# Performance work log

Hardware: AMD Instinct MI355X
Metric: run time of the kernel (lower is better)

The kernel has to match this reference:

```python
import jax, jax.numpy as jnp
import numpy as np

B, C, EMB, W, H = 4, 128, 16, 64, 64


def setup_inputs() -> dict:
    key = jax.random.key(0)
    ks = jax.random.split(key, 8)
    return {
        "x": jax.random.normal(ks[0], (B, C, W, H), dtype=jnp.float32),
        "Wq": jax.random.normal(ks[1], (EMB, C), dtype=jnp.float32) * (1.0 / np.sqrt(C)),
        "bq": jax.random.normal(ks[2], (EMB,), dtype=jnp.float32) * 0.01,
        "Wk": jax.random.normal(ks[3], (EMB, C), dtype=jnp.float32) * (1.0 / np.sqrt(C)),
        "bk": jax.random.normal(ks[4], (EMB,), dtype=jnp.float32) * 0.01,
        "Wv": jax.random.normal(ks[5], (C, C), dtype=jnp.float32) * (1.0 / np.sqrt(C)),
        "bv": jax.random.normal(ks[6], (C,), dtype=jnp.float32) * 0.01,
        "gamma": jax.random.normal(ks[7], (1,), dtype=jnp.float32),
    }


def reference(x, Wq, bq, Wk, bk, Wv, bv, gamma):
    b, c, w, h = x.shape
    n = w * h
    xf = x.reshape(b, c, n)  # flatten spatial: [b, c, n]
    # 1x1 convs == per-pixel linear maps
    q = jnp.einsum('ec,bcn->bne', Wq, xf) + bq                # [b, n, emb]
    k = jnp.einsum('ec,bcn->ben', Wk, xf) + bk[:, None]       # [b, emb, n]
    energy = jnp.einsum('bne,bem->bnm', q, k)                 # [b, n, n] (unscaled)
    attn = jax.nn.softmax(energy, axis=-1)                    # softmax over keys m
    v = jnp.einsum('dc,bcn->bdn', Wv, xf) + bv[:, None]       # [b, c, n]
    # torch: out = bmm(V, attn^T) -> out[b,d,n] = sum_m V[b,d,m] * attn[b,n,m]
    out = jnp.einsum('bdm,bnm->bdn', v, attn)
    out = (gamma * out + xf).reshape(b, c, w, h)
    return out
```

## Files before the change

kernel.cpp:

```cpp
#include <hip/hip_runtime.h>


#define NTILE 64
#define PEXP(s) exp2f(fmaf((s), 1.44269504f, -23.08312065f))

typedef __attribute__((ext_vector_type(8))) short bf16x8;
typedef __attribute__((ext_vector_type(4))) float f32x4;
typedef __attribute__((ext_vector_type(4))) int i32x4;

__device__ __forceinline__ bf16x8 asbf(i32x4 v) {
  return __builtin_bit_cast(bf16x8, v);
}
__device__ __forceinline__ int cvtpk(float lo, float hi) {
  int r;
  asm("v_cvt_pk_bf16_f32 %0, %1, %2" : "=v"(r) : "v"(lo), "v"(hi));
  return r;
}
__device__ __forceinline__ float lo16f(int u) {
  return __uint_as_float(((unsigned)u) << 16);
}
__device__ __forceinline__ float hi16f(int u) {
  return __uint_as_float(((unsigned)u) & 0xffff0000u);
}


__global__ __launch_bounds__(256, 4) void proj_kernel(
    const float* __restrict__ xg, const float* __restrict__ Wq,
    const float* __restrict__ bq, const float* __restrict__ Wk,
    const float* __restrict__ bk, const float* __restrict__ Wv,
    const float* __restrict__ bv, char* __restrict__ Qg,
    char* __restrict__ Kg, char* __restrict__ Vg) {
  __shared__ float wlds[10240];
  const int bid = blockIdx.x;
  const int pt = bid & 127, dh = (bid >> 7) & 1, b = bid >> 8;
  const int n0 = pt << 5;
  const int tid = threadIdx.x;

  const float* Wqk = dh ? Wk : Wq;
  for (int i = tid; i < 2560; i += 256) {
    int row = i >> 5, c4 = (i & 31) << 2;
    const float* src = (row < 64) ? (Wv + (size_t)(dh * 64 + row) * 128 + c4)
                                  : (Wqk + (size_t)(row - 64) * 128 + c4);
    *(f32x4*)&wlds[row * 128 + c4] = *(const f32x4*)src;
  }
  __syncthreads();

  const int px = tid & 31, og = tid >> 5;
  const float* xb = xg + (size_t)b * 524288 + n0 + px;

  float av[8];
#pragma unroll
  for (int r = 0; r < 8; r++) av[r] = 0.f;
  float aq[4] = {0.f, 0.f, 0.f, 0.f};

  for (int c0 = 0; c0 < 128; c0 += 4) {
    float x0 = xb[(size_t)(c0 + 0) * 4096];
    float x1 = xb[(size_t)(c0 + 1) * 4096];
    float x2 = xb[(size_t)(c0 + 2) * 4096];
    float x3 = xb[(size_t)(c0 + 3) * 4096];
#pragma unroll
    for (int r = 0; r < 8; r++) {
      const float* wr = &wlds[(og * 8 + r) * 128 + c0];
      av[r] += wr[0] * x0 + wr[1] * x1 + wr[2] * x2 + wr[3] * x3;
    }
    if (og < 4) {
#pragma unroll
      for (int ee = 0; ee < 4; ee++) {
        const float* wr = &wlds[(64 + og * 4 + ee) * 128 + c0];
        aq[ee] += wr[0] * x0 + wr[1] * x1 + wr[2] * x2 + wr[3] * x3;
      }
    }
  }

  if (og < 4) {
    const float* bqk = dh ? bk : bq;
    float v0 = aq[0] + bqk[og * 4 + 0], v1 = aq[1] + bqk[og * 4 + 1];
    float v2 = aq[2] + bqk[og * 4 + 2], v3 = aq[3] + bqk[og * 4 + 3];
    int h0 = cvtpk(v0, v1), h1 = cvtpk(v2, v3);
    float r0 = v0 - lo16f(h0), r1 = v1 - hi16f(h0);
    float r2 = v2 - lo16f(h1), r3 = v3 - hi16f(h1);
    int l0 = cvtpk(r0, r1), l1 = cvtpk(r2, r3);
    i32x4 ch = {h0, h1, l0, l1};
    char* QKg = dh ? Kg : Qg;
    *(i32x4*)(QKg + ((size_t)(b * 16384 + og * 4096 + n0 + px)) * 16) = ch;
  }

  const int d0 = dh * 64 + og * 8;
#pragma unroll
  for (int r = 0; r < 8; r++) av[r] += bv[d0 + r];
  __syncthreads();
#pragma unroll
  for (int r = 0; r < 8; r++) wlds[(og * 8 + r) * 32 + px] = av[r];
  __syncthreads();

  char* vg_t = Vg + (size_t)b * 2097152 + (size_t)(pt >> 1) * 32768;
#pragma unroll
  for (int k = 0; k < 2; k++) {
    int pid = tid + k * 256;
    int gs = pid & 3, d1 = (pid >> 2) & 63, kcl = pid >> 8;
    int d = dh * 64 + d1;
    int gg = gs ^ ((d >> 1) & 3);
    f32x4 v = *(const f32x4*)&wlds[d1 * 32 + kcl * 16 + gg * 4];
    int h0 = cvtpk(v[0], v[1]), h1 = cvtpk(v[2], v[3]);
    float r0 = v[0] - lo16f(h0), r1 = v[1] - hi16f(h0);
    float r2 = v[2] - lo16f(h1), r3 = v[3] - hi16f(h1);
    int l0 = cvtpk(r0, r1), l1 = cvtpk(r2, r3);
    i32x4 ch = {h0, h1, l0, l1};
    int kc = (pt & 1) * 2 + kcl;
    *(i32x4*)(vg_t + ((size_t)((kc * 128 + d) * 4 + gs)) * 16) = ch;
  }
}

__global__ __launch_bounds__(512, 2) void flash_kernel(
    const char* __restrict__ Qg, const char* __restrict__ Kg,
    const char* __restrict__ Vg, const float* __restrict__ xg,
    const float* __restrict__ gammag, float* __restrict__ outg) {
  __shared__ float red_O[64 * 129];
  __shared__ float red_L[64];

  const int bid = blockIdx.x;
  const int xcd = bid & 7, slot2 = bid >> 3;
  const int b = xcd >> 1;
  const int nt = (slot2 << 1) | (xcd & 1);
  const int n0 = nt << 6;

  const int tid = threadIdx.x;
  const int l = tid & 63, w = tid >> 6;
  const int c = l & 15, g = l >> 4;
  const int kc = w & 3, dh = w >> 2;

  const char* kg_b = Kg + (size_t)b * 262144;
  const char* vg_b = Vg + (size_t)b * 2097152;

  const char* vlane =
      vg_b + ((size_t)(kc * 512 + dh * 256 + c * 4 + (g ^ ((c >> 1) & 3)))) * 16;

  const int krow = kc * 16 + c;
  i32x4 kcur = *(const i32x4*)(kg_b + ((size_t)(g * 4096 + krow)) * 16);
  i32x4 qf[4];
#pragma unroll
  for (int qt = 0; qt < 4; qt++) {
    int n = n0 + qt * 16 + c;
    qf[qt] = *(const i32x4*)(Qg + ((size_t)(b * 16384 + g * 4096 + n)) * 16);
  }

  i32x4 vc0 = *(const i32x4*)(vlane + 0);
  i32x4 vc1 = *(const i32x4*)(vlane + 1024);
  i32x4 vc2 = *(const i32x4*)(vlane + 2048);
  i32x4 vc3 = *(const i32x4*)(vlane + 3072);

  const f32x4 zero4 = {0.f, 0.f, 0.f, 0.f};
  f32x4 acc[4][4];
#pragma unroll
  for (int qt = 0; qt < 4; qt++)
#pragma unroll
    for (int dt = 0; dt < 4; dt++) acc[qt][dt] = zero4;
  float lsum[4] = {0.f, 0.f, 0.f, 0.f};

  for (int t = 0; t < NTILE; t++) {
    i32x4 knext = kcur, vn0 = vc0, vn1 = vc1, vn2 = vc2, vn3 = vc3;
    if (t + 1 < NTILE) {
      const char* vnb = vlane + (size_t)(t + 1) * 32768;
      vn0 = *(const i32x4*)(vnb + 0);
      vn1 = *(const i32x4*)(vnb + 1024);
      vn2 = *(const i32x4*)(vnb + 2048);
      vn3 = *(const i32x4*)(vnb + 3072);
      knext = *(const i32x4*)(kg_b +
                              ((size_t)(g * 4096 + (t + 1) * 64 + krow)) * 16);
    }

    i32x4 k2 = {kcur[2], kcur[3], kcur[0], kcur[1]};
    f32x4 st[4];
    __builtin_amdgcn_s_setprio(1);
#pragma unroll
    for (int qt = 0; qt < 4; qt++) {
      f32x4 s = __builtin_amdgcn_mfma_f32_16x16x32_bf16(asbf(kcur), asbf(qf[qt]),
                                                        zero4, 0, 0, 0);
      st[qt] = __builtin_amdgcn_mfma_f32_16x16x32_bf16(asbf(k2), asbf(qf[qt]), s,
                                                       0, 0, 0);
    }
    __builtin_amdgcn_s_setprio(0);

    bf16x8 af[4];
#pragma unroll
    for (int qt = 0; qt < 4; qt++) {
      float p0 = PEXP(st[qt][0]);
      float p1 = PEXP(st[qt][1]);
      float p2 = PEXP(st[qt][2]);
      float p3 = PEXP(st[qt][3]);
      lsum[qt] += (p0 + p1) + (p2 + p3);
      int h0 = cvtpk(p0, p1), h1 = cvtpk(p2, p3);
      i32x4 A = {h0, h1, h0, h1};
      af[qt] = asbf(A);
    }

    __builtin_amdgcn_s_setprio(1);
#pragma unroll
    for (int qt = 0; qt < 4; qt++) {
      acc[qt][0] = __builtin_amdgcn_mfma_f32_16x16x32_bf16(af[qt], asbf(vc0),
                                                           acc[qt][0], 0, 0, 0);
      acc[qt][1] = __builtin_amdgcn_mfma_f32_16x16x32_bf16(af[qt], asbf(vc1),
                                                           acc[qt][1], 0, 0, 0);
      acc[qt][2] = __builtin_amdgcn_mfma_f32_16x16x32_bf16(af[qt], asbf(vc2),
                                                           acc[qt][2], 0, 0, 0);
      acc[qt][3] = __builtin_amdgcn_mfma_f32_16x16x32_bf16(af[qt], asbf(vc3),
                                                           acc[qt][3], 0, 0, 0);
    }
    __builtin_amdgcn_s_setprio(0);

    kcur = knext;
    vc0 = vn0; vc1 = vn1; vc2 = vn2; vc3 = vn3;
  }

  for (int i = tid; i < 64 * 129; i += 512) red_O[i] = 0.f;
  if (tid < 64) red_L[tid] = 0.f;
  __syncthreads();

#pragma unroll
  for (int qt = 0; qt < 4; qt++) {
    float s = lsum[qt];
    s += __shfl_xor(s, 16);
    s += __shfl_xor(s, 32);
    if (g == 0 && dh == 0) atomicAdd(&red_L[qt * 16 + c], s);
#pragma unroll
    for (int dt = 0; dt < 4; dt++) {
#pragma unroll
      for (int i = 0; i < 4; i++) {
        atomicAdd(&red_O[(qt * 16 + 4 * g + i) * 129 + dh * 64 + dt * 16 + c],
                  acc[qt][dt][i]);
      }
    }
  }
  __syncthreads();

  const float gam = gammag[0];
#pragma unroll
  for (int k = 0; k < 4; k++) {
    int id = tid + k * 512;
    int q4 = id & 15, d = id >> 4;
    int q0 = q4 * 4;
    size_t base = ((size_t)(b * 128 + d)) * 4096 + n0 + q0;
    f32x4 x4 = *(const f32x4*)(xg + base);
    f32x4 o;
#pragma unroll
    for (int j = 0; j < 4; j++)
      o[j] = gam * (red_O[(q0 + j) * 129 + d] / red_L[q0 + j]) + x4[j];
    *(f32x4*)(outg + base) = o;
  }
}

extern "C" void kernel_launch(void* const* d_in, const int* in_sizes, int n_in,
                              void* d_out, int out_size, void* d_ws, size_t ws_size,
                              hipStream_t stream) {
  (void)in_sizes; (void)n_in; (void)out_size; (void)ws_size;
  const float* x = (const float*)d_in[0];
  const float* Wq = (const float*)d_in[1];
  const float* bq = (const float*)d_in[2];
  const float* Wk = (const float*)d_in[3];
  const float* bk = (const float*)d_in[4];
  const float* Wv = (const float*)d_in[5];
  const float* bv = (const float*)d_in[6];
  const float* gamma = (const float*)d_in[7];
  float* out = (float*)d_out;

  char* Qg = (char*)d_ws;
  char* Kg = Qg + (1 << 20);
  char* Vg = Kg + (1 << 20);

  proj_kernel<<<1024, 256, 0, stream>>>(x, Wq, bq, Wk, bk, Wv, bv, Qg, Kg, Vg);
  flash_kernel<<<256, 512, 0, stream>>>(Qg, Kg, Vg, x, gamma, out);
}
```

Before: 205.4 us.

## Halve flash query tile, double-buffer K/V loads, stage proj inputs via async LDS

The flash kernel now handles 32 queries per block instead of 64, launching 512 blocks with a higher occupancy bound. Its K/V register loads are double-buffered across two unrolled tile sets to hide global latency. The projection kernel now stages x and the weights into LDS with async global-to-LDS loads, processes 64 pixels per block and drops the idle Q/K waves. The aim is to fill more CUs and overlap memory latency, at the cost of reading K/V twice as often in total and doing more per-block reduction work.

```diff
diff --git a/kernel.cpp b/kernel.cpp
--- a/kernel.cpp
+++ b/kernel.cpp
@@ -1,7 +1,6 @@
 #include <hip/hip_runtime.h>
 
 
-#define NTILE 64
 #define PEXP(s) exp2f(fmaf((s), 1.44269504f, -23.08312065f))
 
 typedef __attribute__((ext_vector_type(8))) short bf16x8;
@@ -22,57 +21,70 @@
 __device__ __forceinline__ float hi16f(int u) {
   return __uint_as_float(((unsigned)u) & 0xffff0000u);
 }
-
-
-__global__ __launch_bounds__(256, 4) void proj_kernel(
+__device__ __forceinline__ void async16(const void* g, void* l) {
+  __builtin_amdgcn_global_load_lds(
+      (const __attribute__((address_space(1))) void*)g,
+      (__attribute__((address_space(3))) void*)l, 16, 0, 0);
+}
+
+
+__global__ __launch_bounds__(256, 2) void proj_kernel(
     const float* __restrict__ xg, const float* __restrict__ Wq,
     const float* __restrict__ bq, const float* __restrict__ Wk,
     const float* __restrict__ bk, const float* __restrict__ Wv,
     const float* __restrict__ bv, char* __restrict__ Qg,
     char* __restrict__ Kg, char* __restrict__ Vg) {
-  __shared__ float wlds[10240];
+  __shared__ __align__(16) float xl[8192];
+  __shared__ __align__(16) float wl[10240];
   const int bid = blockIdx.x;
-  const int pt = bid & 127, dh = (bid >> 7) & 1, b = bid >> 8;
-  const int n0 = pt << 5;
+  const int xcd = bid & 7, b = xcd >> 1, dh = xcd & 1, pt = bid >> 3;
+  const int n0 = pt << 6;
   const int tid = threadIdx.x;
 
   const float* Wqk = dh ? Wk : Wq;
-  for (int i = tid; i < 2560; i += 256) {
-    int row = i >> 5, c4 = (i & 31) << 2;
-    const float* src = (row < 64) ? (Wv + (size_t)(dh * 64 + row) * 128 + c4)
-                                  : (Wqk + (size_t)(row - 64) * 128 + c4);
-    *(f32x4*)&wlds[row * 128 + c4] = *(const f32x4*)src;
-  }
-  __syncthreads();
-
-  const int px = tid & 31, og = tid >> 5;
-  const float* xb = xg + (size_t)b * 524288 + n0 + px;
-
-  float av[8];
-#pragma unroll
-  for (int r = 0; r < 8; r++) av[r] = 0.f;
+#pragma unroll
+  for (int k = 0; k < 8; k++) {
+    int idx = tid + k * 256;
+    int cc = idx >> 4, p4 = (idx & 15) << 2;
+    const float* src = xg + ((size_t)(b * 128 + cc)) * 4096 + n0 + p4;
+    async16(src, (char*)xl + idx * 16);
+  }
+#pragma unroll
+  for (int k = 0; k < 10; k++) {
+    int j = tid + k * 256;
+    int row = j >> 5, c4 = (j & 31) * 4;
+    const float* src = (k < 8) ? (Wv + (size_t)(dh * 64 + row) * 128 + c4)
+                               : (Wqk + (size_t)(row - 64) * 128 + c4);
+    async16(src, (char*)wl + j * 16);
+  }
+  asm volatile("s_waitcnt vmcnt(0)" ::: "memory");
+  __syncthreads();
+
+  const int px = tid & 63, og = tid >> 6;
+
+  float av[16];
+#pragma unroll
+  for (int i = 0; i < 16; i++) av[i] = 0.f;
   float aq[4] = {0.f, 0.f, 0.f, 0.f};
 
   for (int c0 = 0; c0 < 128; c0 += 4) {
-    float x0 = xb[(size_t)(c0 + 0) * 4096];
-    float x1 = xb[(size_t)(c0 + 1) * 4096];
-    float x2 = xb[(size_t)(c0 + 2) * 4096];
-    float x3 = xb[(size_t)(c0 + 3) * 4096];
-#pragma unroll
-    for (int r = 0; r < 8; r++) {
-      const float* wr = &wlds[(og * 8 + r) * 128 + c0];
+    float x0 = xl[(c0 + 0) * 64 + px];
+    float x1 = xl[(c0 + 1) * 64 + px];
+    float x2 = xl[(c0 + 2) * 64 + px];
+    float x3 = xl[(c0 + 3) * 64 + px];
+#pragma unroll
+    for (int r = 0; r < 16; r++) {
+      const float* wr = &wl[(og * 16 + r) * 128 + c0];
       av[r] += wr[0] * x0 + wr[1] * x1 + wr[2] * x2 + wr[3] * x3;
     }
-    if (og < 4) {
-#pragma unroll
-      for (int ee = 0; ee < 4; ee++) {
-        const float* wr = &wlds[(64 + og * 4 + ee) * 128 + c0];
-        aq[ee] += wr[0] * x0 + wr[1] * x1 + wr[2] * x2 + wr[3] * x3;
-      }
-    }
-  }
-
-  if (og < 4) {
+#pragma unroll
+    for (int ee = 0; ee < 4; ee++) {
+      const float* wr = &wl[(64 + og * 4 + ee) * 128 + c0];
+      aq[ee] += wr[0] * x0 + wr[1] * x1 + wr[2] * x2 + wr[3] * x3;
+    }
+  }
+
+  {
     const float* bqk = dh ? bk : bq;
     float v0 = aq[0] + bqk[og * 4 + 0], v1 = aq[1] + bqk[og * 4 + 1];
     float v2 = aq[2] + bqk[og * 4 + 2], v3 = aq[3] + bqk[og * 4 + 3];
@@ -85,44 +97,101 @@
     *(i32x4*)(QKg + ((size_t)(b * 16384 + og * 4096 + n0 + px)) * 16) = ch;
   }
 
-  const int d0 = dh * 64 + og * 8;
-#pragma unroll
-  for (int r = 0; r < 8; r++) av[r] += bv[d0 + r];
-  __syncthreads();
-#pragma unroll
-  for (int r = 0; r < 8; r++) wlds[(og * 8 + r) * 32 + px] = av[r];
-  __syncthreads();
-
-  char* vg_t = Vg + (size_t)b * 2097152 + (size_t)(pt >> 1) * 32768;
-#pragma unroll
-  for (int k = 0; k < 2; k++) {
-    int pid = tid + k * 256;
-    int gs = pid & 3, d1 = (pid >> 2) & 63, kcl = pid >> 8;
+  const int d0 = dh * 64 + og * 16;
+  __syncthreads();
+#pragma unroll
+  for (int r = 0; r < 16; r++) xl[(og * 16 + r) * 64 + px] = av[r] + bv[d0 + r];
+  __syncthreads();
+
+  char* vg_t = Vg + (size_t)b * 2097152 + (size_t)pt * 32768;
+#pragma unroll
+  for (int k = 0; k < 4; k++) {
+    int id = tid + k * 256;
+    int gs = id & 3, d1 = (id >> 2) & 63, kc = id >> 8;
     int d = dh * 64 + d1;
     int gg = gs ^ ((d >> 1) & 3);
-    f32x4 v = *(const f32x4*)&wlds[d1 * 32 + kcl * 16 + gg * 4];
+    f32x4 v = *(const f32x4*)&xl[d1 * 64 + kc * 16 + gg * 4];
     int h0 = cvtpk(v[0], v[1]), h1 = cvtpk(v[2], v[3]);
     float r0 = v[0] - lo16f(h0), r1 = v[1] - hi16f(h0);
     float r2 = v[2] - lo16f(h1), r3 = v[3] - hi16f(h1);
     int l0 = cvtpk(r0, r1), l1 = cvtpk(r2, r3);
     i32x4 ch = {h0, h1, l0, l1};
-    int kc = (pt & 1) * 2 + kcl;
     *(i32x4*)(vg_t + ((size_t)((kc * 128 + d) * 4 + gs)) * 16) = ch;
   }
 }
 
-__global__ __launch_bounds__(512, 2) void flash_kernel(
+#define COMPUTE(KF, V0, V1, V2, V3)                                            \
+  {                                                                            \
+    i32x4 k2 = {KF[2], KF[3], KF[0], KF[1]};                                   \
+    __builtin_amdgcn_s_setprio(1);                                             \
+    f32x4 s0 = __builtin_amdgcn_mfma_f32_16x16x32_bf16(asbf(KF), asbf(qf0),    \
+                                                       zero4, 0, 0, 0);        \
+    s0 = __builtin_amdgcn_mfma_f32_16x16x32_bf16(asbf(k2), asbf(qf0), s0, 0,   \
+                                                 0, 0);                        \
+    f32x4 s1 = __builtin_amdgcn_mfma_f32_16x16x32_bf16(asbf(KF), asbf(qf1),    \
+                                                       zero4, 0, 0, 0);        \
+    s1 = __builtin_amdgcn_mfma_f32_16x16x32_bf16(asbf(k2), asbf(qf1), s1, 0,   \
+                                                 0, 0);                        \
+    __builtin_amdgcn_s_setprio(0);                                             \
+    bf16x8 a0, a1;                                                             \
+    {                                                                          \
+      float p0 = PEXP(s0[0]), p1 = PEXP(s0[1]), p2 = PEXP(s0[2]),              \
+            p3 = PEXP(s0[3]);                                                  \
+      lsum0 += (p0 + p1) + (p2 + p3);                                          \
+      int h0 = cvtpk(p0, p1), h1 = cvtpk(p2, p3);                              \
+      i32x4 A = {h0, h1, h0, h1};                                              \
+      a0 = asbf(A);                                                            \
+    }                                                                          \
+    {                                                                          \
+      float p0 = PEXP(s1[0]), p1 = PEXP(s1[1]), p2 = PEXP(s1[2]),              \
+            p3 = PEXP(s1[3]);                                                  \
+      lsum1 += (p0 + p1) + (p2 + p3);                                          \
+      int h0 = cvtpk(p0, p1), h1 = cvtpk(p2, p3);                              \
+      i32x4 A = {h0, h1, h0, h1};                                              \
+      a1 = asbf(A);                                                            \
+    }                                                                          \
+    __builtin_amdgcn_s_setprio(1);                                             \
+    acc[0][0] = __builtin_amdgcn_mfma_f32_16x16x32_bf16(a0, asbf(V0),          \
+                                                        acc[0][0], 0, 0, 0);   \
+    acc[0][1] = __builtin_amdgcn_mfma_f32_16x16x32_bf16(a0, asbf(V1),          \
+                                                        acc[0][1], 0, 0, 0);   \
+    acc[0][2] = __builtin_amdgcn_mfma_f32_16x16x32_bf16(a0, asbf(V2),          \
+                                                        acc[0][2], 0, 0, 0);   \
+    acc[0][3] = __builtin_amdgcn_mfma_f32_16x16x32_bf16(a0, asbf(V3),          \
+                                                        acc[0][3], 0, 0, 0);   \
+    acc[1][0] = __builtin_amdgcn_mfma_f32_16x16x32_bf16(a1, asbf(V0),          \
+                                                        acc[1][0], 0, 0, 0);   \
+    acc[1][1] = __builtin_amdgcn_mfma_f32_16x16x32_bf16(a1, asbf(V1),          \
+                                                        acc[1][1], 0, 0, 0);   \
+    acc[1][2] = __builtin_amdgcn_mfma_f32_16x16x32_bf16(a1, asbf(V2),          \
+                                                        acc[1][2], 0, 0, 0);   \
+    acc[1][3] = __builtin_amdgcn_mfma_f32_16x16x32_bf16(a1, asbf(V3),          \
+                                                        acc[1][3], 0, 0, 0);   \
+    __builtin_amdgcn_s_setprio(0);                                             \
+  }
+
+#define LOADSET(KF, V0, V1, V2, V3, tt)                                        \
+  {                                                                            \
+    const char* vp = vlane + (size_t)(tt)*32768;                               \
+    V0 = *(const i32x4*)(vp);                                                  \
+    V1 = *(const i32x4*)(vp + 1024);                                           \
+    V2 = *(const i32x4*)(vp + 2048);                                           \
+    V3 = *(const i32x4*)(vp + 3072);                                           \
+    KF = *(const i32x4*)(kg_b + ((size_t)(g * 4096 + (tt)*64 + krow)) * 16);   \
+  }
+
+__global__ __launch_bounds__(512, 4) void flash_kernel(
     const char* __restrict__ Qg, const char* __restrict__ Kg,
     const char* __restrict__ Vg, const float* __restrict__ xg,
     const float* __restrict__ gammag, float* __restrict__ outg) {
-  __shared__ float red_O[64 * 129];
-  __shared__ float red_L[64];
+  __shared__ float red_O[32 * 129];
+  __shared__ float red_L[32];
 
   const int bid = blockIdx.x;
-  const int xcd = bid & 7, slot2 = bid >> 3;
+  const int xcd = bid & 7;
   const int b = xcd >> 1;
-  const int nt = (slot2 << 1) | (xcd & 1);
-  const int n0 = nt << 6;
+  const int nt = ((bid >> 3) << 1) | (xcd & 1);
+  const int n0 = nt << 5;
 
   const int tid = threadIdx.x;
   const int l = tid & 63, w = tid >> 6;
@@ -131,97 +200,57 @@
 
   const char* kg_b = Kg + (size_t)b * 262144;
   const char* vg_b = Vg + (size_t)b * 2097152;
-
   const char* vlane =
       vg_b + ((size_t)(kc * 512 + dh * 256 + c * 4 + (g ^ ((c >> 1) & 3)))) * 16;
-
   const int krow = kc * 16 + c;
-  i32x4 kcur = *(const i32x4*)(kg_b + ((size_t)(g * 4096 + krow)) * 16);
-  i32x4 qf[4];
-#pragma unroll
-  for (int qt = 0; qt < 4; qt++) {
-    int n = n0 + qt * 16 + c;
-    qf[qt] = *(const i32x4*)(Qg + ((size_t)(b * 16384 + g * 4096 + n)) * 16);
-  }
-
-  i32x4 vc0 = *(const i32x4*)(vlane + 0);
-  i32x4 vc1 = *(const i32x4*)(vlane + 1024);
-  i32x4 vc2 = *(const i32x4*)(vlane + 2048);
-  i32x4 vc3 = *(const i32x4*)(vlane + 3072);
+
+  const i32x4 qf0 =
+      *(const i32x4*)(Qg + ((size_t)(b * 16384 + g * 4096 + n0 + c)) * 16);
+  const i32x4 qf1 =
+      *(const i32x4*)(Qg + ((size_t)(b * 16384 + g * 4096 + n0 + 16 + c)) * 16);
 
   const f32x4 zero4 = {0.f, 0.f, 0.f, 0.f};
-  f32x4 acc[4][4];
-#pragma unroll
-  for (int qt = 0; qt < 4; qt++)
+  f32x4 acc[2][4];
+#pragma unroll
+  for (int qt = 0; qt < 2; qt++)
 #pragma unroll
     for (int dt = 0; dt < 4; dt++) acc[qt][dt] = zero4;
-  float lsum[4] = {0.f, 0.f, 0.f, 0.f};
-
-  for (int t = 0; t < NTILE; t++) {
-    i32x4 knext = kcur, vn0 = vc0, vn1 = vc1, vn2 = vc2, vn3 = vc3;
-    if (t + 1 < NTILE) {
-      const char* vnb = vlane + (size_t)(t + 1) * 32768;
-      vn0 = *(const i32x4*)(vnb + 0);
-      vn1 = *(const i32x4*)(vnb + 1024);
-      vn2 = *(const i32x4*)(vnb + 2048);
-      vn3 = *(const i32x4*)(vnb + 3072);
-      knext = *(const i32x4*)(kg_b +
-                              ((size_t)(g * 4096 + (t + 1) * 64 + krow)) * 16);
-    }
-
-    i32x4 k2 = {kcur[2], kcur[3], kcur[0], kcur[1]};
-    f32x4 st[4];
-    __builtin_amdgcn_s_setprio(1);
-#pragma unroll
-    for (int qt = 0; qt < 4; qt++) {
-      f32x4 s = __builtin_amdgcn_mfma_f32_16x16x32_bf16(asbf(kcur), asbf(qf[qt]),
-                                                        zero4, 0, 0, 0);
-      st[qt] = __builtin_amdgcn_mfma_f32_16x16x32_bf16(asbf(k2), asbf(qf[qt]), s,
-                                                       0, 0, 0);
-    }
-    __builtin_amdgcn_s_setprio(0);
-
-    bf16x8 af[4];
-#pragma unroll
-    for (int qt = 0; qt < 4; qt++) {
-      float p0 = PEXP(st[qt][0]);
-      float p1 = PEXP(st[qt][1]);
-      float p2 = PEXP(st[qt][2]);
-      float p3 = PEXP(st[qt][3]);
-      lsum[qt] += (p0 + p1) + (p2 + p3);
-      int h0 = cvtpk(p0, p1), h1 = cvtpk(p2, p3);
-      i32x4 A = {h0, h1, h0, h1};
-      af[qt] = asbf(A);
-    }
-
-    __builtin_amdgcn_s_setprio(1);
-#pragma unroll
-    for (int qt = 0; qt < 4; qt++) {
-      acc[qt][0] = __builtin_amdgcn_mfma_f32_16x16x32_bf16(af[qt], asbf(vc0),
-                                                           acc[qt][0], 0, 0, 0);
-      acc[qt][1] = __builtin_amdgcn_mfma_f32_16x16x32_bf16(af[qt], asbf(vc1),
-                                                           acc[qt][1], 0, 0, 0);
-      acc[qt][2] = __builtin_amdgcn_mfma_f32_16x16x32_bf16(af[qt], asbf(vc2),
-                                                           acc[qt][2], 0, 0, 0);
-      acc[qt][3] = __builtin_amdgcn_mfma_f32_16x16x32_bf16(af[qt], asbf(vc3),
-                                                           acc[qt][3], 0, 0, 0);
-    }
-    __builtin_amdgcn_s_setprio(0);
-
-    kcur = knext;
-    vc0 = vn0; vc1 = vn1; vc2 = vn2; vc3 = vn3;
-  }
-
-  for (int i = tid; i < 64 * 129; i += 512) red_O[i] = 0.f;
-  if (tid < 64) red_L[tid] = 0.f;
-  __syncthreads();
-
-#pragma unroll
-  for (int qt = 0; qt < 4; qt++) {
-    float s = lsum[qt];
+  float lsum0 = 0.f, lsum1 = 0.f;
+
+  i32x4 ka, va0, va1, va2, va3;
+  i32x4 kb, vb0, vb1, vb2, vb3;
+  LOADSET(ka, va0, va1, va2, va3, 0);
+  LOADSET(kb, vb0, vb1, vb2, vb3, 1);
+
+  for (int t = 0; t < 64; t += 2) {
+    COMPUTE(ka, va0, va1, va2, va3);
+    {
+      int t2 = (t + 2 < 64) ? t + 2 : 63;
+      LOADSET(ka, va0, va1, va2, va3, t2);
+    }
+    COMPUTE(kb, vb0, vb1, vb2, vb3);
+    {
+      int t3 = (t + 3 < 64) ? t + 3 : 63;
+      LOADSET(kb, vb0, vb1, vb2, vb3, t3);
+    }
+  }
+
+  for (int i = tid; i < 32 * 129; i += 512) red_O[i] = 0.f;
+  if (tid < 32) red_L[tid] = 0.f;
+  __syncthreads();
+
+  {
+    float s = lsum0;
     s += __shfl_xor(s, 16);
     s += __shfl_xor(s, 32);
-    if (g == 0 && dh == 0) atomicAdd(&red_L[qt * 16 + c], s);
+    if (g == 0 && dh == 0) atomicAdd(&red_L[c], s);
+    s = lsum1;
+    s += __shfl_xor(s, 16);
+    s += __shfl_xor(s, 32);
+    if (g == 0 && dh == 0) atomicAdd(&red_L[16 + c], s);
+  }
+#pragma unroll
+  for (int qt = 0; qt < 2; qt++) {
 #pragma unroll
     for (int dt = 0; dt < 4; dt++) {
 #pragma unroll
@@ -235,9 +264,9 @@
 
   const float gam = gammag[0];
 #pragma unroll
-  for (int k = 0; k < 4; k++) {
+  for (int k = 0; k < 2; k++) {
     int id = tid + k * 512;
-    int q4 = id & 15, d = id >> 4;
+    int q4 = id & 7, d = id >> 3;
     int q0 = q4 * 4;
     size_t base = ((size_t)(b * 128 + d)) * 4096 + n0 + q0;
     f32x4 x4 = *(const f32x4*)(xg + base);
@@ -267,6 +296,6 @@
   char* Kg = Qg + (1 << 20);
   char* Vg = Kg + (1 << 20);
 
-  proj_kernel<<<1024, 256, 0, stream>>>(x, Wq, bq, Wk, bk, Wv, bv, Qg, Kg, Vg);
-  flash_kernel<<<256, 512, 0, stream>>>(Qg, Kg, Vg, x, gamma, out);
-}
+  proj_kernel<<<512, 256, 0, stream>>>(x, Wq, bq, Wk, bk, Wv, bv, Qg, Kg, Vg);
+  flash_kernel<<<512, 512, 0, stream>>>(Qg, Kg, Vg, x, gamma, out);
+}
```

Result: faster. 182.3 us (-11.3%).
